# Optimization experiments

Hardware: AMD Instinct MI355X
Metric: run time of the kernel (lower is better)

## Reference

```python
import jax, jax.numpy as jnp
import numpy as np

N_NODES = 10000
N_EDGES = 16384
D = 128            # node_in_dim == out_dim == edge_attr_dim == hidden_dim


def setup_inputs() -> dict:
    key = jax.random.key(0)
    ks = jax.random.split(key, 9)
    s = 1.0 / np.sqrt(D)
    x = jax.random.normal(ks[0], (N_NODES, D), dtype=jnp.float32)
    edge_index = jax.random.randint(ks[1], (2, N_EDGES), 0, N_NODES, dtype=jnp.int64)
    edge_attr = jax.random.normal(ks[2], (N_EDGES, D), dtype=jnp.float32)
    # edge_net: MLP 128 -> 128 (ReLU) -> 128*128
    w1 = jax.random.normal(ks[3], (D, D), dtype=jnp.float32) * s
    b1 = jnp.zeros((D,), dtype=jnp.float32)
    w2 = jax.random.normal(ks[4], (D, D * D), dtype=jnp.float32) * s
    b2 = jnp.zeros((D * D,), dtype=jnp.float32)
    # NNConv root weight and bias
    root = jax.random.normal(ks[5], (D, D), dtype=jnp.float32) * s
    bias = jnp.zeros((D,), dtype=jnp.float32)
    return {"x": x, "edge_index": edge_index, "edge_attr": edge_attr,
            "w1": w1, "b1": b1, "w2": w2, "b2": b2, "root": root, "bias": bias}


def reference(x, edge_index, edge_attr, w1, b1, w2, b2, root, bias):
    src, dst = edge_index[0], edge_index[1]
    # edge_net -> per-edge weight matrices [E, D, D]
    h = jax.nn.relu(edge_attr @ w1 + b1)
    w_edge = (h @ w2 + b2).reshape(-1, D, D)
    # gather source features, per-edge matvec: [E, D]
    x_j = x[src]
    msg = jnp.einsum('ei,eio->eo', x_j, w_edge)
    # scatter-mean into destination nodes
    seg_sum = jax.ops.segment_sum(msg, dst, num_segments=N_NODES)
    cnt = jax.ops.segment_sum(jnp.ones((msg.shape[0],), msg.dtype), dst,
                              num_segments=N_NODES)
    aggr = seg_sum / jnp.maximum(cnt, 1.0)[:, None]
    # NNConv root transform + bias
    conv_out = aggr + x @ root + bias
    # residual + exact GELU (torch nn.GELU default)
    return x + jax.nn.gelu(conv_out, approximate=False)
```

## Files before the change

### kernel.cpp

```cpp
#include <hip/hip_runtime.h>
#include <math.h>

#define D 128
#define NNODES 10000
#define NEDGES 16384
#define PADR 136
#define MAXDEG 16

typedef short short8 __attribute__((ext_vector_type(8)));
typedef float floatx4 __attribute__((ext_vector_type(4)));

__device__ __forceinline__ float bf2f(unsigned short u) {
  union { unsigned u; float f; } v; v.u = ((unsigned)u) << 16; return v.f;
}
__device__ __forceinline__ unsigned short f2bf(float f) {
  union { float f; unsigned u; } v; v.f = f;
  return (unsigned short)((v.u + 0x7FFFu + ((v.u >> 16) & 1u)) >> 16);
}
__device__ __forceinline__ float bflo(unsigned u) {
  union { unsigned u; float f; } v; v.u = u << 16; return v.f;
}
__device__ __forceinline__ float bfhi(unsigned u) {
  union { unsigned u; float f; } v; v.u = u & 0xFFFF0000u; return v.f;
}
__device__ __forceinline__ short8 pack8(float4 a, float4 b) {
  short8 r;
  r[0] = (short)f2bf(a.x); r[1] = (short)f2bf(a.y);
  r[2] = (short)f2bf(a.z); r[3] = (short)f2bf(a.w);
  r[4] = (short)f2bf(b.x); r[5] = (short)f2bf(b.y);
  r[6] = (short)f2bf(b.z); r[7] = (short)f2bf(b.w);
  return r;
}

__global__ __launch_bounds__(256) void k2_prep(
    const float* __restrict__ w2, const float* __restrict__ b2,
    const float* __restrict__ w1, const float* __restrict__ root,
    unsigned short* __restrict__ w2t, unsigned short* __restrict__ w1t,
    unsigned short* __restrict__ rootT) {
  __shared__ float L[32][129];
  const int t = threadIdx.x;
  const int bid = blockIdx.x;
  const float* __restrict__ src;
  unsigned short* dst;
  int o0;
  if (bid < 516) {
    const int k = bid >> 2;
    o0 = (bid & 3) * 32;
    src = (k < D) ? (w2 + (long)k * (D * D)) : b2;
    dst = w2t + (long)k * (D * PADR);
  } else if (bid < 520) {
    o0 = (bid - 516) * 32; src = w1; dst = w1t;
  } else {
    o0 = (bid - 520) * 32; src = root; dst = rootT;
  }
#pragma unroll
  for (int r = 0; r < 16; ++r) {
    int idx = r * 256 + t;
    int i = idx >> 5, oc = idx & 31;
    L[oc][i] = src[i * D + o0 + oc];
  }
  __syncthreads();
#pragma unroll
  for (int r = 0; r < 8; ++r) {
    int p = r * 256 + t;
    int oc = p >> 6, i2 = (p & 63) * 2;
    unsigned v = (unsigned)f2bf(L[oc][i2]) | ((unsigned)f2bf(L[oc][i2 + 1]) << 16);
    *(unsigned*)(dst + ((o0 + oc) * PADR + i2)) = v;
  }
}

__global__ __launch_bounds__(256) void k1_edge(
    const float* __restrict__ x, const int* __restrict__ eidx,
    const float* __restrict__ ea, const unsigned short* __restrict__ w1t,
    const float* __restrict__ b1, unsigned short* __restrict__ hT,
    unsigned short* __restrict__ xjb, int* __restrict__ cnt,
    int* __restrict__ elist) {
  const int t = threadIdx.x;
  const int e0 = blockIdx.x * 64;
  if (t < 64) {
    const int e = e0 + t;
    const int d = eidx[NEDGES + e];
    const int pos = atomicAdd(&cnt[d], 1);
    if (pos < MAXDEG) elist[d * MAXDEG + pos] = e;
  }
#pragma unroll 4
  for (int r = 0; r < 16; ++r) {
    int idx = r * 256 + t, e = idx >> 6, i2 = (idx & 63) * 2;
    const int s = eidx[e0 + e];
    const float2 v = *(const float2*)(x + (long)s * D + i2);
    unsigned p = (unsigned)f2bf(v.x) | ((unsigned)f2bf(v.y) << 16);
    *(unsigned*)(xjb + ((e0 + e) * PADR + i2)) = p;
  }
  const int lane = t & 63, w = t >> 6, lo = lane & 15, hi = lane >> 4;
  short8 af[4];
#pragma unroll
  for (int ks = 0; ks < 4; ++ks) {
    const float* p0 = ea + (long)(e0 + w * 16 + lo) * D + ks * 32 + hi * 8;
    af[ks] = pack8(*(const float4*)p0, *(const float4*)(p0 + 4));
  }
  floatx4 acc[8];
#pragma unroll
  for (int nt = 0; nt < 8; ++nt) acc[nt] = (floatx4){0.f, 0.f, 0.f, 0.f};
#pragma unroll
  for (int ks = 0; ks < 4; ++ks) {
    const int ib = ks * 32 + hi * 8;
#pragma unroll
    for (int nt = 0; nt < 8; ++nt) {
      const short8 bf_ = *(const short8*)&w1t[(nt * 16 + lo) * PADR + ib];
      acc[nt] = __builtin_amdgcn_mfma_f32_16x16x32_bf16(af[ks], bf_, acc[nt], 0, 0, 0);
    }
  }
#pragma unroll
  for (int nt = 0; nt < 8; ++nt) {
    const int ko = nt * 16 + lo;
    const float b1v = b1[ko];
    float v0 = fmaxf(acc[nt][0] + b1v, 0.f);
    float v1 = fmaxf(acc[nt][1] + b1v, 0.f);
    float v2 = fmaxf(acc[nt][2] + b1v, 0.f);
    float v3 = fmaxf(acc[nt][3] + b1v, 0.f);
    uint2 pk;
    pk.x = (unsigned)f2bf(v0) | ((unsigned)f2bf(v1) << 16);
    pk.y = (unsigned)f2bf(v2) | ((unsigned)f2bf(v3) << 16);
    *(uint2*)(hT + (ko * NEDGES + e0 + w * 16 + hi * 4)) = pk;
  }
  if (t < 64) hT[128 * NEDGES + e0 + t] = 0x3F80;
}

__global__ __launch_bounds__(256, 3) void k3_msg(
    const unsigned short* __restrict__ w2t,
    const unsigned short* __restrict__ xjb,
    const unsigned short* __restrict__ hT,
    unsigned short* __restrict__ msgout) {
  __shared__ float hLT[65 * 128];
  const int t = threadIdx.x;
  const int b = blockIdx.x;
  const int kh = b & 1;
  const int oq = (b >> 1) & 3;
  const int eg = b >> 3;
  const int e0 = eg * 128;
  const int o0 = oq * 32;
  const int kbase = kh * 64;
  const int kcnt = kh ? 65 : 64;
  const int lane = t & 63, wv = t >> 6;
  const int lo = lane & 15, hi = lane >> 4;
  const int we = (wv >> 1) * 64;
  const int wo = (wv & 1) * 16;

  for (int idx = t; idx < kcnt * 64; idx += 256) {
    const int kk = idx >> 6, e2 = (idx & 63) * 2;
    const unsigned u = *(const unsigned*)&hT[(long)(kbase + kk) * NEDGES + e0 + e2];
    const int ebase = kk * 128;
#pragma unroll
    for (int q = 0; q < 2; ++q) {
      const int e = e2 + q;
      hLT[ebase + ((e >> 6) << 6) + ((e & 15) << 2) + ((e >> 4) & 3)] =
          q ? bfhi(u) : bflo(u);
    }
  }

  short8 xf[4][4];
#pragma unroll
  for (int ne = 0; ne < 4; ++ne)
#pragma unroll
    for (int ks = 0; ks < 4; ++ks)
      xf[ne][ks] = *(const short8*)&xjb[(long)(e0 + we + ne * 16 + lo) * PADR + ks * 32 + hi * 8];
  __syncthreads();

  const long kstride = (long)D * PADR;
  const unsigned short* ap = w2t + (long)kbase * kstride + (long)(o0 + wo + lo) * PADR + hi * 8;
  const float* hp = hLT + we + lo * 4;
  short8 a0[4], a1[4];
#pragma unroll
  for (int ks = 0; ks < 4; ++ks) a0[ks] = *(const short8*)(ap + ks * 32);
#pragma unroll
  for (int ks = 0; ks < 4; ++ks) a1[ks] = *(const short8*)(ap + kstride + ks * 32);
  floatx4 msg[4];
#pragma unroll
  for (int ne = 0; ne < 4; ++ne) msg[ne] = (floatx4){0.f, 0.f, 0.f, 0.f};

  auto body = [&](short8* fr, int k) {
    const floatx4 h4 = *(const floatx4*)(hp + k * 128);
    floatx4 P[4];
#pragma unroll
    for (int ne = 0; ne < 4; ++ne) P[ne] = (floatx4){0.f, 0.f, 0.f, 0.f};
#pragma unroll
    for (int ks = 0; ks < 4; ++ks)
#pragma unroll
      for (int ne = 0; ne < 4; ++ne)
        P[ne] = __builtin_amdgcn_mfma_f32_16x16x32_bf16(fr[ks], xf[ne][ks], P[ne], 0, 0, 0);
#pragma unroll
    for (int ne = 0; ne < 4; ++ne)
#pragma unroll
      for (int r = 0; r < 4; ++r) msg[ne][r] += h4[ne] * P[ne][r];
  };

  const int kpairs = kcnt >> 1;
  for (int j = 0; j < kpairs; ++j) {
    const int k = j * 2;
    body(a0, k);
    {
      const int kp = (k + 2 < kcnt) ? k + 2 : 0;
#pragma unroll
      for (int ks = 0; ks < 4; ++ks)
        a0[ks] = *(const short8*)(ap + (long)kp * kstride + ks * 32);
    }
    body(a1, k + 1);
    {
      const int kp = (k + 3 < kcnt) ? k + 3 : 0;
#pragma unroll
      for (int ks = 0; ks < 4; ++ks)
        a1[ks] = *(const short8*)(ap + (long)kp * kstride + ks * 32);
    }
  }
  if (kcnt & 1) body(a0, kcnt - 1);

#pragma unroll
  for (int ne = 0; ne < 4; ++ne) {
    const long e = e0 + we + ne * 16 + lo;
    uint2 pk;
    pk.x = (unsigned)f2bf(msg[ne][0]) | ((unsigned)f2bf(msg[ne][1]) << 16);
    pk.y = (unsigned)f2bf(msg[ne][2]) | ((unsigned)f2bf(msg[ne][3]) << 16);
    *(uint2*)(msgout + ((long)kh * NEDGES + e) * D + o0 + wo + hi * 4) = pk;
  }
}

__global__ __launch_bounds__(256) void k4_out(
    const float* __restrict__ x, const unsigned short* __restrict__ rootT,
    const float* __restrict__ bias, const unsigned short* __restrict__ msg,
    const int* __restrict__ cnt, const int* __restrict__ elist,
    float* __restrict__ out) {
  __shared__ float segL[64 * 132];
  const int t = threadIdx.x;
  const int n0 = blockIdx.x * 64;
  {
    const int ln = t >> 2;
    const int n = n0 + ln;
    const int oq = (t & 3) * 32;
    float a[32];
#pragma unroll
    for (int i = 0; i < 32; ++i) a[i] = 0.f;
    if (n < NNODES) {
      const int deg = min(cnt[n], MAXDEG);
      for (int j = 0; j < deg; ++j) {
        const int e = elist[n * MAXDEG + j];
        const unsigned short* r0 = msg + (long)e * D + oq;
        const unsigned short* r1 = r0 + (long)NEDGES * D;
#pragma unroll
        for (int q = 0; q < 4; ++q) {
          const uint4 u0 = *(const uint4*)(r0 + q * 8);
          const uint4 u1 = *(const uint4*)(r1 + q * 8);
          a[q * 8 + 0] += bflo(u0.x) + bflo(u1.x);
          a[q * 8 + 1] += bfhi(u0.x) + bfhi(u1.x);
          a[q * 8 + 2] += bflo(u0.y) + bflo(u1.y);
          a[q * 8 + 3] += bfhi(u0.y) + bfhi(u1.y);
          a[q * 8 + 4] += bflo(u0.z) + bflo(u1.z);
          a[q * 8 + 5] += bfhi(u0.z) + bfhi(u1.z);
          a[q * 8 + 6] += bflo(u0.w) + bflo(u1.w);
          a[q * 8 + 7] += bfhi(u0.w) + bfhi(u1.w);
        }
      }
    }
#pragma unroll
    for (int q = 0; q < 8; ++q)
      *(float4*)&segL[ln * 132 + oq + q * 4] =
          (float4){a[q * 4], a[q * 4 + 1], a[q * 4 + 2], a[q * 4 + 3]};
  }
  __syncthreads();
  const int lane = t & 63, w = t >> 6, lo = lane & 15, hi = lane >> 4;
  const int nrow = n0 + w * 16 + lo;
  short8 af[4];
#pragma unroll
  for (int ks = 0; ks < 4; ++ks) {
    if (nrow < NNODES) {
      const float* p0 = x + (long)nrow * D + ks * 32 + hi * 8;
      af[ks] = pack8(*(const float4*)p0, *(const float4*)(p0 + 4));
    } else {
      af[ks] = (short8){0, 0, 0, 0, 0, 0, 0, 0};
    }
  }
  floatx4 acc[8];
#pragma unroll
  for (int nt = 0; nt < 8; ++nt) acc[nt] = (floatx4){0.f, 0.f, 0.f, 0.f};
#pragma unroll
  for (int ks = 0; ks < 4; ++ks) {
    const int ib = ks * 32 + hi * 8;
#pragma unroll
    for (int nt = 0; nt < 8; ++nt) {
      const short8 bf_ = *(const short8*)&rootT[(nt * 16 + lo) * PADR + ib];
      acc[nt] = __builtin_amdgcn_mfma_f32_16x16x32_bf16(af[ks], bf_, acc[nt], 0, 0, 0);
    }
  }
  float dinv[4];
#pragma unroll
  for (int r = 0; r < 4; ++r) {
    const int n = n0 + w * 16 + hi * 4 + r;
    dinv[r] = (n < NNODES) ? 1.0f / fmaxf((float)cnt[n], 1.0f) : 0.f;
  }
#pragma unroll
  for (int nt = 0; nt < 8; ++nt) {
    const int co = nt * 16 + lo;
    const float bv = bias[co];
#pragma unroll
    for (int r = 0; r < 4; ++r) {
      const int n = n0 + w * 16 + hi * 4 + r;
      if (n < NNODES) {
        const float aggr = segL[(w * 16 + hi * 4 + r) * 132 + co] * dinv[r];
        const float v = acc[nt][r] + aggr + bv;
        const float ge = 0.5f * v * (1.0f + erff(v * 0.70710678f));
        out[(long)n * D + co] = x[(long)n * D + co] + ge;
      }
    }
  }
}

extern "C" void kernel_launch(void* const* d_in, const int* in_sizes, int n_in,
                              void* d_out, int out_size, void* d_ws, size_t ws_size,
                              hipStream_t stream) {
  (void)in_sizes; (void)n_in; (void)out_size; (void)ws_size;
  const float* x    = (const float*)d_in[0];
  const int*   eidx = (const int*)d_in[1];
  const float* ea   = (const float*)d_in[2];
  const float* w1   = (const float*)d_in[3];
  const float* b1   = (const float*)d_in[4];
  const float* w2   = (const float*)d_in[5];
  const float* b2   = (const float*)d_in[6];
  const float* root = (const float*)d_in[7];
  const float* bias = (const float*)d_in[8];
  float* out = (float*)d_out;
  char* ws = (char*)d_ws;
  unsigned short* hT    = (unsigned short*)(ws + 0);
  unsigned short* xjb   = (unsigned short*)(ws + 4227072);
  unsigned short* w2t   = (unsigned short*)(ws + 8683520);
  unsigned short* msg   = (unsigned short*)(ws + 13174784);
  int*            cnt   = (int*)(ws + 21563392);
  int*            elist = (int*)(ws + 21603392);
  unsigned short* w1t   = (unsigned short*)(ws + 22243392);
  unsigned short* rootT = (unsigned short*)(ws + 22278208);
  hipMemsetAsync(cnt, 0, 40000, stream);
  hipLaunchKernelGGL(k2_prep, dim3(524), dim3(256), 0, stream,
                     w2, b2, w1, root, w2t, w1t, rootT);
  hipLaunchKernelGGL(k1_edge, dim3(NEDGES / 64), dim3(256), 0, stream,
                     x, eidx, ea, w1t, b1, hT, xjb, cnt, elist);
  hipLaunchKernelGGL(k3_msg, dim3(1024), dim3(256), 0, stream,
                     w2t, xjb, hT, msg);
  hipLaunchKernelGGL(k4_out, dim3((NNODES + 63) / 64), dim3(256), 0, stream,
                     x, rootT, bias, msg, cnt, elist, out);
}
```

Baseline: 185.3 us.

## Store hidden activations as fp32 and read them directly from global in msg kernel

The edge MLP hidden activations are now written as fp32 in transposed layout. The message kernel drops its LDS staging and sync and loads per-k h values straight from global into registers, prefetched alongside the w2 fragments. The count memset is folded into the prep kernel as extra blocks, and the launch-bounds occupancy hint is removed. This removes the LDS fill and barrier at the cost of doubling the hT buffer footprint and issuing scattered scalar global loads inside the k loop.

```diff
diff --git a/kernel.cpp b/kernel.cpp
--- a/kernel.cpp
+++ b/kernel.cpp
@@ -36,10 +36,15 @@
     const float* __restrict__ w2, const float* __restrict__ b2,
     const float* __restrict__ w1, const float* __restrict__ root,
     unsigned short* __restrict__ w2t, unsigned short* __restrict__ w1t,
-    unsigned short* __restrict__ rootT) {
+    unsigned short* __restrict__ rootT, int* __restrict__ cnt) {
   __shared__ float L[32][129];
   const int t = threadIdx.x;
   const int bid = blockIdx.x;
+  if (bid >= 524) {
+    const int i = (bid - 524) * 256 + t;
+    if (i < NNODES) cnt[i] = 0;
+    return;
+  }
   const float* __restrict__ src;
   unsigned short* dst;
   int o0;
@@ -72,7 +77,7 @@
 __global__ __launch_bounds__(256) void k1_edge(
     const float* __restrict__ x, const int* __restrict__ eidx,
     const float* __restrict__ ea, const unsigned short* __restrict__ w1t,
-    const float* __restrict__ b1, unsigned short* __restrict__ hT,
+    const float* __restrict__ b1, float* __restrict__ hTf,
     unsigned short* __restrict__ xjb, int* __restrict__ cnt,
     int* __restrict__ elist) {
   const int t = threadIdx.x;
@@ -114,24 +119,21 @@
   for (int nt = 0; nt < 8; ++nt) {
     const int ko = nt * 16 + lo;
     const float b1v = b1[ko];
-    float v0 = fmaxf(acc[nt][0] + b1v, 0.f);
-    float v1 = fmaxf(acc[nt][1] + b1v, 0.f);
-    float v2 = fmaxf(acc[nt][2] + b1v, 0.f);
-    float v3 = fmaxf(acc[nt][3] + b1v, 0.f);
-    uint2 pk;
-    pk.x = (unsigned)f2bf(v0) | ((unsigned)f2bf(v1) << 16);
-    pk.y = (unsigned)f2bf(v2) | ((unsigned)f2bf(v3) << 16);
-    *(uint2*)(hT + (ko * NEDGES + e0 + w * 16 + hi * 4)) = pk;
-  }
-  if (t < 64) hT[128 * NEDGES + e0 + t] = 0x3F80;
-}
-
-__global__ __launch_bounds__(256, 3) void k3_msg(
+    float4 v;
+    v.x = fmaxf(acc[nt][0] + b1v, 0.f);
+    v.y = fmaxf(acc[nt][1] + b1v, 0.f);
+    v.z = fmaxf(acc[nt][2] + b1v, 0.f);
+    v.w = fmaxf(acc[nt][3] + b1v, 0.f);
+    *(float4*)&hTf[(long)ko * NEDGES + e0 + w * 16 + hi * 4] = v;
+  }
+  if (t < 64) hTf[(long)128 * NEDGES + e0 + t] = 1.0f;
+}
+
+__global__ __launch_bounds__(256) void k3_msg(
     const unsigned short* __restrict__ w2t,
     const unsigned short* __restrict__ xjb,
-    const unsigned short* __restrict__ hT,
+    const float* __restrict__ hTf,
     unsigned short* __restrict__ msgout) {
-  __shared__ float hLT[65 * 128];
   const int t = threadIdx.x;
   const int b = blockIdx.x;
   const int kh = b & 1;
@@ -146,40 +148,31 @@
   const int we = (wv >> 1) * 64;
   const int wo = (wv & 1) * 16;
 
-  for (int idx = t; idx < kcnt * 64; idx += 256) {
-    const int kk = idx >> 6, e2 = (idx & 63) * 2;
-    const unsigned u = *(const unsigned*)&hT[(long)(kbase + kk) * NEDGES + e0 + e2];
-    const int ebase = kk * 128;
-#pragma unroll
-    for (int q = 0; q < 2; ++q) {
-      const int e = e2 + q;
-      hLT[ebase + ((e >> 6) << 6) + ((e & 15) << 2) + ((e >> 4) & 3)] =
-          q ? bfhi(u) : bflo(u);
-    }
-  }
-
   short8 xf[4][4];
 #pragma unroll
   for (int ne = 0; ne < 4; ++ne)
 #pragma unroll
     for (int ks = 0; ks < 4; ++ks)
       xf[ne][ks] = *(const short8*)&xjb[(long)(e0 + we + ne * 16 + lo) * PADR + ks * 32 + hi * 8];
-  __syncthreads();
 
   const long kstride = (long)D * PADR;
   const unsigned short* ap = w2t + (long)kbase * kstride + (long)(o0 + wo + lo) * PADR + hi * 8;
-  const float* hp = hLT + we + lo * 4;
+  const float* hp = hTf + (long)kbase * NEDGES + e0 + we + lo;
   short8 a0[4], a1[4];
+  float h0[4], h1[4];
 #pragma unroll
   for (int ks = 0; ks < 4; ++ks) a0[ks] = *(const short8*)(ap + ks * 32);
 #pragma unroll
   for (int ks = 0; ks < 4; ++ks) a1[ks] = *(const short8*)(ap + kstride + ks * 32);
+#pragma unroll
+  for (int ne = 0; ne < 4; ++ne) h0[ne] = hp[ne * 16];
+#pragma unroll
+  for (int ne = 0; ne < 4; ++ne) h1[ne] = hp[NEDGES + ne * 16];
   floatx4 msg[4];
 #pragma unroll
   for (int ne = 0; ne < 4; ++ne) msg[ne] = (floatx4){0.f, 0.f, 0.f, 0.f};
 
-  auto body = [&](short8* fr, int k) {
-    const floatx4 h4 = *(const floatx4*)(hp + k * 128);
+  auto body = [&](short8* fr, float* hk) {
     floatx4 P[4];
 #pragma unroll
     for (int ne = 0; ne < 4; ++ne) P[ne] = (floatx4){0.f, 0.f, 0.f, 0.f};
@@ -191,28 +184,31 @@
 #pragma unroll
     for (int ne = 0; ne < 4; ++ne)
 #pragma unroll
-      for (int r = 0; r < 4; ++r) msg[ne][r] += h4[ne] * P[ne][r];
+      for (int r = 0; r < 4; ++r) msg[ne][r] += hk[ne] * P[ne][r];
   };
 
-  const int kpairs = kcnt >> 1;
-  for (int j = 0; j < kpairs; ++j) {
+  for (int j = 0; j < 32; ++j) {
     const int k = j * 2;
-    body(a0, k);
+    body(a0, h0);
     {
       const int kp = (k + 2 < kcnt) ? k + 2 : 0;
 #pragma unroll
       for (int ks = 0; ks < 4; ++ks)
         a0[ks] = *(const short8*)(ap + (long)kp * kstride + ks * 32);
-    }
-    body(a1, k + 1);
+#pragma unroll
+      for (int ne = 0; ne < 4; ++ne) h0[ne] = hp[(long)kp * NEDGES + ne * 16];
+    }
+    body(a1, h1);
     {
       const int kp = (k + 3 < kcnt) ? k + 3 : 0;
 #pragma unroll
       for (int ks = 0; ks < 4; ++ks)
         a1[ks] = *(const short8*)(ap + (long)kp * kstride + ks * 32);
-    }
-  }
-  if (kcnt & 1) body(a0, kcnt - 1);
+#pragma unroll
+      for (int ne = 0; ne < 4; ++ne) h1[ne] = hp[(long)kp * NEDGES + ne * 16];
+    }
+  }
+  if (kcnt & 1) body(a0, h0);
 
 #pragma unroll
   for (int ne = 0; ne < 4; ++ne) {
@@ -328,21 +324,20 @@
   const float* bias = (const float*)d_in[8];
   float* out = (float*)d_out;
   char* ws = (char*)d_ws;
-  unsigned short* hT    = (unsigned short*)(ws + 0);
-  unsigned short* xjb   = (unsigned short*)(ws + 4227072);
-  unsigned short* w2t   = (unsigned short*)(ws + 8683520);
-  unsigned short* msg   = (unsigned short*)(ws + 13174784);
-  int*            cnt   = (int*)(ws + 21563392);
-  int*            elist = (int*)(ws + 21603392);
-  unsigned short* w1t   = (unsigned short*)(ws + 22243392);
-  unsigned short* rootT = (unsigned short*)(ws + 22278208);
-  hipMemsetAsync(cnt, 0, 40000, stream);
-  hipLaunchKernelGGL(k2_prep, dim3(524), dim3(256), 0, stream,
-                     w2, b2, w1, root, w2t, w1t, rootT);
+  float*          hTf   = (float*)(ws + 0);
+  unsigned short* xjb   = (unsigned short*)(ws + 8454144);
+  unsigned short* w2t   = (unsigned short*)(ws + 12910592);
+  unsigned short* msg   = (unsigned short*)(ws + 17401856);
+  int*            cnt   = (int*)(ws + 25790464);
+  int*            elist = (int*)(ws + 25830464);
+  unsigned short* w1t   = (unsigned short*)(ws + 26470464);
+  unsigned short* rootT = (unsigned short*)(ws + 26505280);
+  hipLaunchKernelGGL(k2_prep, dim3(564), dim3(256), 0, stream,
+                     w2, b2, w1, root, w2t, w1t, rootT, cnt);
   hipLaunchKernelGGL(k1_edge, dim3(NEDGES / 64), dim3(256), 0, stream,
-                     x, eidx, ea, w1t, b1, hT, xjb, cnt, elist);
+                     x, eidx, ea, w1t, b1, hTf, xjb, cnt, elist);
   hipLaunchKernelGGL(k3_msg, dim3(1024), dim3(256), 0, stream,
-                     w2t, xjb, hT, msg);
+                     w2t, xjb, hTf, msg);
   hipLaunchKernelGGL(k4_out, dim3((NNODES + 63) / 64), dim3(256), 0, stream,
                      x, rootT, bias, msg, cnt, elist, out);
 }
```

After: 194.8 us. 5.1% more time.

## Store hidden activations as bf16 in LDS, raise k3 occupancy, fold memset into prep

Applied to the files above, without the earlier changes.

In the message kernel the staged per-edge hidden activations are kept as bf16 in shared memory instead of fp32, and are unpacked to float on each load. This halves the LDS footprint, which lets the launch bound rise to 4 blocks per CU for more latency hiding. The k-loop trip count is now a compile-time constant, and the hipMemsetAsync of the count array is replaced by extra blocks in the prep kernel, saving one launch. Extra unpack ALU work and register pressure at the higher occupancy target may offset part of the gain.

```diff
diff --git a/kernel.cpp b/kernel.cpp
--- a/kernel.cpp
+++ b/kernel.cpp
@@ -36,10 +36,15 @@
     const float* __restrict__ w2, const float* __restrict__ b2,
     const float* __restrict__ w1, const float* __restrict__ root,
     unsigned short* __restrict__ w2t, unsigned short* __restrict__ w1t,
-    unsigned short* __restrict__ rootT) {
+    unsigned short* __restrict__ rootT, int* __restrict__ cnt) {
   __shared__ float L[32][129];
   const int t = threadIdx.x;
   const int bid = blockIdx.x;
+  if (bid >= 524) {
+    const int i = (bid - 524) * 256 + t;
+    if (i < NNODES) cnt[i] = 0;
+    return;
+  }
   const float* __restrict__ src;
   unsigned short* dst;
   int o0;
@@ -126,12 +131,12 @@
   if (t < 64) hT[128 * NEDGES + e0 + t] = 0x3F80;
 }
 
-__global__ __launch_bounds__(256, 3) void k3_msg(
+__global__ __launch_bounds__(256, 4) void k3_msg(
     const unsigned short* __restrict__ w2t,
     const unsigned short* __restrict__ xjb,
     const unsigned short* __restrict__ hT,
     unsigned short* __restrict__ msgout) {
-  __shared__ float hLT[65 * 128];
+  __shared__ unsigned short hLT[65 * 128];
   const int t = threadIdx.x;
   const int b = blockIdx.x;
   const int kh = b & 1;
@@ -150,12 +155,11 @@
     const int kk = idx >> 6, e2 = (idx & 63) * 2;
     const unsigned u = *(const unsigned*)&hT[(long)(kbase + kk) * NEDGES + e0 + e2];
     const int ebase = kk * 128;
-#pragma unroll
-    for (int q = 0; q < 2; ++q) {
-      const int e = e2 + q;
-      hLT[ebase + ((e >> 6) << 6) + ((e & 15) << 2) + ((e >> 4) & 3)] =
-          q ? bfhi(u) : bflo(u);
-    }
+    const int e1 = e2 + 1;
+    hLT[ebase + ((e2 >> 6) << 6) + ((e2 & 15) << 2) + ((e2 >> 4) & 3)] =
+        (unsigned short)(u & 0xFFFFu);
+    hLT[ebase + ((e1 >> 6) << 6) + ((e1 & 15) << 2) + ((e1 >> 4) & 3)] =
+        (unsigned short)(u >> 16);
   }
 
   short8 xf[4][4];
@@ -168,7 +172,7 @@
 
   const long kstride = (long)D * PADR;
   const unsigned short* ap = w2t + (long)kbase * kstride + (long)(o0 + wo + lo) * PADR + hi * 8;
-  const float* hp = hLT + we + lo * 4;
+  const unsigned short* hp = hLT + we + lo * 4;
   short8 a0[4], a1[4];
 #pragma unroll
   for (int ks = 0; ks < 4; ++ks) a0[ks] = *(const short8*)(ap + ks * 32);
@@ -179,7 +183,10 @@
   for (int ne = 0; ne < 4; ++ne) msg[ne] = (floatx4){0.f, 0.f, 0.f, 0.f};
 
   auto body = [&](short8* fr, int k) {
-    const floatx4 h4 = *(const floatx4*)(hp + k * 128);
+    const uint2 hu = *(const uint2*)(hp + k * 128);
+    float h4[4];
+    h4[0] = bflo(hu.x); h4[1] = bfhi(hu.x);
+    h4[2] = bflo(hu.y); h4[3] = bfhi(hu.y);
     floatx4 P[4];
 #pragma unroll
     for (int ne = 0; ne < 4; ++ne) P[ne] = (floatx4){0.f, 0.f, 0.f, 0.f};
@@ -194,8 +201,7 @@
       for (int r = 0; r < 4; ++r) msg[ne][r] += h4[ne] * P[ne][r];
   };
 
-  const int kpairs = kcnt >> 1;
-  for (int j = 0; j < kpairs; ++j) {
+  for (int j = 0; j < 32; ++j) {
     const int k = j * 2;
     body(a0, k);
     {
@@ -212,7 +218,7 @@
         a1[ks] = *(const short8*)(ap + (long)kp * kstride + ks * 32);
     }
   }
-  if (kcnt & 1) body(a0, kcnt - 1);
+  if (kcnt & 1) body(a0, 64);
 
 #pragma unroll
   for (int ne = 0; ne < 4; ++ne) {
@@ -336,9 +342,8 @@
   int*            elist = (int*)(ws + 21603392);
   unsigned short* w1t   = (unsigned short*)(ws + 22243392);
   unsigned short* rootT = (unsigned short*)(ws + 22278208);
-  hipMemsetAsync(cnt, 0, 40000, stream);
-  hipLaunchKernelGGL(k2_prep, dim3(524), dim3(256), 0, stream,
-                     w2, b2, w1, root, w2t, w1t, rootT);
+  hipLaunchKernelGGL(k2_prep, dim3(564), dim3(256), 0, stream,
+                     w2, b2, w1, root, w2t, w1t, rootT, cnt);
   hipLaunchKernelGGL(k1_edge, dim3(NEDGES / 64), dim3(256), 0, stream,
                      x, eidx, ea, w1t, b1, hT, xjb, cnt, elist);
   hipLaunchKernelGGL(k3_msg, dim3(1024), dim3(256), 0, stream,
```

Result: slower. 263.8 us (+42.4%).
